# Kernel optimization log

Hardware: AMD Instinct MI355X
Metric: run time of the kernel (lower is better)

## Reference

```python
import jax, jax.numpy as jnp
import numpy as np

# --- static module config (from init_kwargs) ---
C1_OUT = 64          # c1OutChannels
C1K = 400            # k winners in conv layer
N_FC = 1024          # fc1 hidden units (n)
K_FC = 100           # k winners in fc1
BOOST = 1.0          # boostStrength
W_SPARSITY = 0.5     # weightSparsity: fraction of fc1 weights allowed nonzero
HP = 12              # pooled spatial size: floor((28-5+1)/2)
C1_OUTPUT_LEN = C1_OUT * HP * HP  # 9216
BATCH = 4096


def setup_inputs() -> dict:
    key = jax.random.key(0)
    ks = jax.random.split(key, 10)
    x = jax.random.normal(ks[0], (BATCH, 1, 28, 28), jnp.float32)
    c1_w = jax.random.normal(ks[1], (C1_OUT, 1, 5, 5), jnp.float32) * 0.1
    c1_b = jax.random.normal(ks[2], (C1_OUT,), jnp.float32) * 0.01
    # duty cycles live in [0, ~density]
    duty_cnn = jax.random.uniform(ks[3], (1, C1_OUT, 1, 1), jnp.float32) * 0.05
    fc1_w = jax.random.normal(ks[4], (N_FC, C1_OUT_LEN_ := C1_OUTPUT_LEN), jnp.float32) * 0.01
    fc1_mask_raw = jax.random.uniform(ks[5], (N_FC, C1_OUTPUT_LEN), jnp.float32)
    fc1_b = jax.random.normal(ks[6], (N_FC,), jnp.float32) * 0.01
    duty_fc = jax.random.uniform(ks[7], (N_FC,), jnp.float32) * 0.1
    fc2_w = jax.random.normal(ks[8], (10, N_FC), jnp.float32) * 0.05
    fc2_b = jnp.zeros((10,), jnp.float32)
    return dict(x=x, c1_w=c1_w, c1_b=c1_b, duty_cnn=duty_cnn, fc1_w=fc1_w,
                fc1_mask_raw=fc1_mask_raw, fc1_b=fc1_b, duty_fc=duty_fc,
                fc2_w=fc2_w, fc2_b=fc2_b)


def _kwinners(x_flat, boost_flat, k):
    """Duty-cycle-boosted k-winner mask.
    x_flat: [B, N]; boost_flat: [1, N] broadcastable boost factors.
    Keeps original x values at the top-k boosted positions per row, zeros rest.
    Boosting uses stop_gradient(x), matching KWinners*.forward(x.detach()*boost).
    """
    boosted = jax.lax.stop_gradient(x_flat) * boost_flat
    thr = jax.lax.top_k(boosted, k)[0][:, -1:]  # k-th largest per row
    return jnp.where(boosted >= thr, x_flat, jnp.zeros((), x_flat.dtype))


def reference(x, c1_w, c1_b, duty_cnn, fc1_w, fc1_mask_raw, fc1_b, duty_fc,
              fc2_w, fc2_b):
    B = x.shape[0]
    # conv2d (valid, stride 1) -> [B, 64, 24, 24]
    y = jax.lax.conv_general_dilated(
        x, c1_w, window_strides=(1, 1), padding='VALID',
        dimension_numbers=('NCHW', 'OIHW', 'NCHW')) + c1_b[None, :, None, None]
    # max_pool2d(2) -> [B, 64, 12, 12]
    y = jax.lax.reduce_window(y, -jnp.inf, jax.lax.max,
                              (1, 1, 2, 2), (1, 1, 2, 2), 'VALID')
    # KWinnersCNN: global top-k over flattened (C,H,W), per-channel boost
    target_density = C1K / C1_OUTPUT_LEN
    boost_c = jnp.exp((target_density - duty_cnn) * BOOST)  # [1,C,1,1]
    boost_flat = jnp.broadcast_to(boost_c, (1, C1_OUT, HP, HP)).reshape(1, -1)
    yf = _kwinners(y.reshape(B, -1), boost_flat, C1K)  # [B, 9216]
    # LinearSDR fc1: sparse-weight linear + KWinners
    w_mask = (fc1_mask_raw < W_SPARSITY).astype(fc1_w.dtype)
    h = yf @ (fc1_w * w_mask).T + fc1_b  # [B, 1024]
    boost_fc = jnp.exp((K_FC / N_FC - duty_fc) * BOOST)[None, :]
    h = _kwinners(h, boost_fc, K_FC)
    # fc2 + log_softmax (dropout inactive in eval mode)
    logits = h @ fc2_w.T + fc2_b
    return jax.nn.log_softmax(logits, axis=1)
```

## Files before the change

### kernel.cpp

```cpp
#include <hip/hip_runtime.h>

__device__ __forceinline__ float b2f(unsigned short u) {
  return __uint_as_float(((unsigned)u) << 16);
}
__device__ __forceinline__ unsigned short f2b(float f) {
  unsigned u = __float_as_uint(f);
  return (unsigned short)((u + 0x7FFFu + ((u >> 16) & 1u)) >> 16);
}
__device__ __forceinline__ float gload(const void* p, int i, int isb) {
  return isb ? b2f(((const unsigned short*)p)[i]) : ((const float*)p)[i];
}
__device__ __forceinline__ unsigned tokey(float f) {
  unsigned u = __float_as_uint(f);
  return u ^ (unsigned)(((int)u >> 31) | 0x80000000u);
}

__global__ void k_detect(const void* x, int* flag) {
  int tid = threadIdx.x;
  unsigned short u = ((const unsigned short*)x)[2 * tid];
  int e = (u >> 7) & 0xFF;
  bool sane = (e >= 100 && e <= 140);
  unsigned long long m = __ballot(sane);
  if (tid == 0) *flag = (__popcll(m) >= 40) ? 1 : 0;
}

__global__ __launch_bounds__(256) void k_prep(const void* __restrict__ fc1w,
                                              const void* __restrict__ mraw,
                                              float* __restrict__ WtF,
                                              const int* __restrict__ flag) {
  __shared__ float tile[64][65];
  const int isb = *flag;
  const int i0 = blockIdx.x * 64;
  const int u0 = blockIdx.y * 64;
  const int tx = threadIdx.x & 63, ty = threadIdx.x >> 6;
  for (int uu = ty; uu < 64; uu += 4) {
    int gi = (u0 + uu) * 9216 + i0 + tx;
    float wv = gload(fc1w, gi, isb);
    float mv = gload(mraw, gi, isb);
    tile[uu][tx] = (mv < 0.5f) ? wv : 0.0f;
  }
  __syncthreads();
  for (int ii = ty; ii < 64; ii += 4)
    WtF[(i0 + ii) * 1024 + u0 + tx] = tile[tx][ii];
}

__global__ __launch_bounds__(256) void k_conv(const void* __restrict__ x,
                                              const void* __restrict__ c1w_g,
                                              const void* __restrict__ c1b_g,
                                              const void* __restrict__ duty_g,
                                              int2* __restrict__ wpair,
                                              int* __restrict__ wcnt,
                                              const int* __restrict__ flag) {
  __shared__ __align__(16) float img[784];
  __shared__ float cw[1600];
  __shared__ float cb[64], bcs[64];
  __shared__ __align__(16) float pooled[9216];
  __shared__ unsigned hist4[4][256];
  __shared__ unsigned wtot[4];
  __shared__ unsigned selb, selk;
  const int tid = threadIdx.x;
  const int b = blockIdx.x;
  const int isb = *flag;
  const int lane = tid & 63;
  const int wv_id = tid >> 6;

  for (int i = tid; i < 784; i += 256) img[i] = gload(x, b * 784 + i, isb);
  for (int i = tid; i < 1600; i += 256) cw[i] = gload(c1w_g, i, isb);
  if (tid < 64) {
    cb[tid] = gload(c1b_g, tid, isb);
    float arg = (float)(400.0 / 9216.0) - gload(duty_g, tid, isb);
    bcs[tid] = (float)exp((double)arg);
  }
  __syncthreads();

  {
    const int c = tid >> 2;
    const int half = tid & 1;
    const int ph0 = ((tid >> 1) & 1) * 6;
    float w[25];
#pragma unroll
    for (int i = 0; i < 25; ++i) w[i] = cw[c * 25 + i];
    const float bias = cb[c];
    float R[6][16];
#pragma unroll
    for (int r = 0; r < 6; ++r) {
      int ir = 2 * ph0 + r;
#pragma unroll
      for (int q = 0; q < 4; ++q)
        ((float4*)&R[r][0])[q] = ((const float4*)img)[ir * 7 + half * 3 + q];
    }
#pragma unroll
    for (int i = 0; i < 6; ++i) {
      const int ph = ph0 + i;
      float a0[12], a1[12];
#pragma unroll
      for (int j = 0; j < 12; ++j) { a0[j] = 0.f; a1[j] = 0.f; }
#pragma unroll
      for (int kj = 0; kj < 5; ++kj) {
#pragma unroll
        for (int kr = 0; kr < 5; ++kr) {
          float wk = w[kr * 5 + kj];
          const float* r0 = &R[(2 * i + kr) % 6][0];
          const float* r1 = &R[(2 * i + kr + 1) % 6][0];
#pragma unroll
          for (int j = 0; j < 12; ++j) {
            a0[j] = fmaf(r0[j + kj], wk, a0[j]);
            a1[j] = fmaf(r1[j + kj], wk, a1[j]);
          }
        }
      }
      int obase = c * 144 + ph * 12 + half * 6;
#pragma unroll
      for (int q = 0; q < 6; ++q) {
        float m = fmaxf(fmaxf(a0[2 * q], a0[2 * q + 1]),
                        fmaxf(a1[2 * q], a1[2 * q + 1]));
        pooled[obase + q] = m + bias;
      }
      if (i < 5) {
        int ir0 = 2 * ph + 6, ir1 = 2 * ph + 7;
        float* d0 = &R[(2 * i) % 6][0];
        float* d1 = &R[(2 * i + 1) % 6][0];
#pragma unroll
        for (int q = 0; q < 4; ++q) {
          ((float4*)d0)[q] = ((const float4*)img)[ir0 * 7 + half * 3 + q];
          ((float4*)d1)[q] = ((const float4*)img)[ir1 * 7 + half * 3 + q];
        }
      }
    }
  }
  __syncthreads();

  unsigned keys[36];
  {
    const float bcf = bcs[tid >> 2];
#pragma unroll
    for (int e4 = 0; e4 < 9; ++e4) {
      float4 pv = ((float4*)pooled)[tid * 9 + e4];
      keys[4 * e4 + 0] = tokey(pv.x * bcf);
      keys[4 * e4 + 1] = tokey(pv.y * bcf);
      keys[4 * e4 + 2] = tokey(pv.z * bcf);
      keys[4 * e4 + 3] = tokey(pv.w * bcf);
    }
  }

  unsigned kfix = 0;
  unsigned kk = 400;
  for (int pass = 3; pass >= 0; --pass) {
    const int shift = pass * 8;
    const unsigned himask = (pass == 3) ? 0u : (0xFFFFFFFFu << (shift + 8));
#pragma unroll
    for (int w2 = 0; w2 < 4; ++w2) hist4[w2][tid] = 0;
    __syncthreads();
    unsigned* myh = hist4[wv_id];
#pragma unroll
    for (int e = 0; e < 36; ++e) {
      unsigned key = keys[e];
      if (((key ^ kfix) & himask) == 0)
        atomicAdd(&myh[(key >> shift) & 255u], 1u);
    }
    __syncthreads();
    unsigned own = hist4[0][tid] + hist4[1][tid] + hist4[2][tid] + hist4[3][tid];
    unsigned v = own;
#pragma unroll
    for (int off = 1; off < 64; off <<= 1) {
      unsigned y = __shfl_down(v, off, 64);
      if (lane + off < 64) v += y;
    }
    if (lane == 0) wtot[wv_id] = v;
    __syncthreads();
#pragma unroll
    for (int w2 = 0; w2 < 4; ++w2)
      if (w2 > wv_id) v += wtot[w2];
    unsigned snext = v - own;
    if (v >= kk && snext < kk) {
      selb = (unsigned)tid;
      selk = kk - snext;
    }
    __syncthreads();
    kfix |= selb << shift;
    kk = selk;
    __syncthreads();
  }

  unsigned mycnt = 0;
#pragma unroll
  for (int e = 0; e < 36; ++e) mycnt += (keys[e] >= kfix) ? 1u : 0u;
  unsigned px = mycnt;
#pragma unroll
  for (int off = 1; off < 64; off <<= 1) {
    unsigned y = __shfl_up(px, off, 64);
    if (lane >= off) px += y;
  }
  if (lane == 63) wtot[wv_id] = px;
  __syncthreads();
  unsigned base = 0;
#pragma unroll
  for (int w2 = 0; w2 < 4; ++w2)
    if (w2 < wv_id) base += wtot[w2];
  int pos = (int)(base + px - mycnt);
  for (int e = 0; e < 36; ++e) {
    if (keys[e] >= kfix) {
      int o = tid * 36 + e;
      if (pos < 512)
        wpair[b * 512 + pos] = make_int2(__float_as_int(pooled[o]), o << 12);
      ++pos;
    }
  }
  if (tid == 0) {
    unsigned tot = wtot[0] + wtot[1] + wtot[2] + wtot[3];
    wcnt[b] = (int)(tot < 512u ? tot : 512u);
  }
}

__global__ __launch_bounds__(128) void k_fc1(const float* __restrict__ WtF,
                                             const int2* __restrict__ wpair,
                                             const int* __restrict__ wcnt,
                                             const void* __restrict__ fc1b,
                                             float* __restrict__ h,
                                             const int* __restrict__ flag) {
  __shared__ int2 wl[512];
  const int tid = threadIdx.x;
  const int img = blockIdx.x >> 3;
  const int slice = blockIdx.x & 7;
  const int isb = *flag;
  const int cnt = wcnt[img];
  const int2* __restrict__ wp = wpair + img * 512;
  for (int i = tid; i < cnt; i += 128) wl[i] = wp[i];
  __syncthreads();
  const int u = (slice << 7) + tid;
  const unsigned ub = (unsigned)u * 4u;
  const char* __restrict__ Wb = (const char*)WtF;
  float acc = 0.f;
#pragma unroll 8
  for (int w = 0; w < cnt; ++w) {
    int2 p = wl[w];
    acc = fmaf(__int_as_float(p.x),
               *(const float*)(Wb + ((unsigned)p.y + ub)), acc);
  }
  h[img * 1024 + u] = acc + gload(fc1b, u, isb);
}

__global__ __launch_bounds__(256) void k_sel(const float* __restrict__ h,
                                             const void* __restrict__ dutyfc,
                                             const void* __restrict__ fc2w,
                                             const void* __restrict__ fc2b,
                                             void* __restrict__ out,
                                             const int* __restrict__ flag) {
  __shared__ unsigned hist[256];
  __shared__ unsigned selb, selk;
  __shared__ double lg[10];
  __shared__ double mred[2];
  const int tid = threadIdx.x;
  const int row = blockIdx.x;
  const int isb = *flag;
  if (tid < 10) lg[tid] = (double)gload(fc2b, tid, isb);
  __syncthreads();

  const int u0 = 2 * tid, u1 = 2 * tid + 1, u2 = 512 + 2 * tid, u3 = 513 + 2 * tid;
  float2 hlo = ((const float2*)(h + row * 1024))[tid];
  float2 hhi = ((const float2*)(h + row * 1024 + 512))[tid];
  float h0 = hlo.x, h1 = hlo.y, h2 = hhi.x, h3 = hhi.y;
  float bf0 = (float)exp((double)(0.09765625f - gload(dutyfc, u0, isb)));
  float bf1 = (float)exp((double)(0.09765625f - gload(dutyfc, u1, isb)));
  float bf2 = (float)exp((double)(0.09765625f - gload(dutyfc, u2, isb)));
  float bf3 = (float)exp((double)(0.09765625f - gload(dutyfc, u3, isb)));
  unsigned k0 = tokey(h0 * bf0);
  unsigned k1 = tokey(h1 * bf1);
  unsigned k2 = tokey(h2 * bf2);
  unsigned k3 = tokey(h3 * bf3);

  unsigned kfix = 0;
  int kk = 100;
  for (int pass = 3; pass >= 0; --pass) {
    const int shift = pass * 8;
    const unsigned himask = (pass == 3) ? 0u : (0xFFFFFFFFu << (shift + 8));
    hist[tid] = 0;
    __syncthreads();
    if (((k0 ^ kfix) & himask) == 0) atomicAdd(&hist[(k0 >> shift) & 255u], 1u);
    if (((k1 ^ kfix) & himask) == 0) atomicAdd(&hist[(k1 >> shift) & 255u], 1u);
    if (((k2 ^ kfix) & himask) == 0) atomicAdd(&hist[(k2 >> shift) & 255u], 1u);
    if (((k3 ^ kfix) & himask) == 0) atomicAdd(&hist[(k3 >> shift) & 255u], 1u);
    __syncthreads();
    unsigned v = hist[tid];
    for (int offs = 1; offs < 256; offs <<= 1) {
      unsigned other = (tid + offs < 256) ? hist[tid + offs] : 0u;
      __syncthreads();
      v += other;
      hist[tid] = v;
      __syncthreads();
    }
    unsigned snext = (tid < 255) ? hist[tid + 1] : 0u;
    if (v >= (unsigned)kk && snext < (unsigned)kk) {
      selb = (unsigned)tid;
      selk = (unsigned)(kk - (int)snext);
    }
    __syncthreads();
    kfix |= selb << shift;
    kk = (int)selk;
    __syncthreads();
  }
  bool kp0 = k0 >= kfix, kp1 = k1 >= kfix, kp2 = k2 >= kfix, kp3 = k3 >= kfix;

  double part[10];
#pragma unroll
  for (int c = 0; c < 10; ++c) part[c] = 0.0;
  if (kp0) {
#pragma unroll
    for (int c = 0; c < 10; ++c) part[c] = fma((double)h0, (double)gload(fc2w, c * 1024 + u0, isb), part[c]);
  }
  if (kp1) {
#pragma unroll
    for (int c = 0; c < 10; ++c) part[c] = fma((double)h1, (double)gload(fc2w, c * 1024 + u1, isb), part[c]);
  }
  if (kp2) {
#pragma unroll
    for (int c = 0; c < 10; ++c) part[c] = fma((double)h2, (double)gload(fc2w, c * 1024 + u2, isb), part[c]);
  }
  if (kp3) {
#pragma unroll
    for (int c = 0; c < 10; ++c) part[c] = fma((double)h3, (double)gload(fc2w, c * 1024 + u3, isb), part[c]);
  }
#pragma unroll
  for (int c = 0; c < 10; ++c) {
    double p = part[c];
    for (int off = 32; off > 0; off >>= 1) p += __shfl_xor(p, off);
    if ((tid & 63) == 0) atomicAdd(&lg[c], p);
  }
  __syncthreads();
  if (tid == 0) {
    double m = lg[0];
#pragma unroll
    for (int c = 1; c < 10; ++c) m = lg[c] > m ? lg[c] : m;
    double sum = 0.0;
#pragma unroll
    for (int c = 0; c < 10; ++c) sum += exp(lg[c] - m);
    mred[0] = m;
    mred[1] = log(sum);
  }
  __syncthreads();
  if (tid < 10) {
    double o = lg[tid] - mred[0] - mred[1];
    if (isb)
      ((unsigned short*)out)[row * 10 + tid] = f2b((float)o);
    else
      ((float*)out)[row * 10 + tid] = (float)o;
  }
}

extern "C" void kernel_launch(void* const* d_in, const int* in_sizes, int n_in,
                              void* d_out, int out_size, void* d_ws, size_t ws_size,
                              hipStream_t stream) {
  char* ws = (char*)d_ws;
  float* WtF = (float*)ws;
  int2* wpair = (int2*)(ws + 37748736);
  int* wcnt = (int*)(ws + 54525952);
  float* h = (float*)(ws + 54542336);
  int* flag = (int*)(ws + 71319552);

  k_detect<<<1, 64, 0, stream>>>(d_in[0], flag);
  k_prep<<<dim3(144, 16), 256, 0, stream>>>(d_in[4], d_in[5], WtF, flag);
  k_conv<<<4096, 256, 0, stream>>>(d_in[0], d_in[1], d_in[2], d_in[3],
                                   wpair, wcnt, flag);
  k_fc1<<<4096 * 8, 128, 0, stream>>>(WtF, wpair, wcnt, d_in[6], h, flag);
  k_sel<<<4096, 256, 0, stream>>>(h, d_in[7], d_in[8], d_in[9], d_out, flag);
}
```

Baseline: 624.5 us.

## Split conv kernel into conv/pool and k-winner selection kernels via global buffer

The fused conv+pool+top-k kernel is split in two. The first computes pooled activations and writes them to a global scratch buffer. The second reads them back, runs the radix-select and writes the winner pairs, processed in four chunks of 1024 images. The aim is to drop the 36KB shared pooled array so more blocks fit per CU, at the cost of an extra global round trip through L2 and more kernel launches. The scratch buffer aliases h, which is safe only because fc1 writes h afterwards.

```diff
diff --git a/kernel.cpp b/kernel.cpp
--- a/kernel.cpp
+++ b/kernel.cpp
@@ -44,102 +44,120 @@
     WtF[(i0 + ii) * 1024 + u0 + tx] = tile[tx][ii];
 }
 
-__global__ __launch_bounds__(256) void k_conv(const void* __restrict__ x,
-                                              const void* __restrict__ c1w_g,
-                                              const void* __restrict__ c1b_g,
-                                              const void* __restrict__ duty_g,
-                                              int2* __restrict__ wpair,
-                                              int* __restrict__ wcnt,
-                                              const int* __restrict__ flag) {
+__global__ __launch_bounds__(256) void k_convA(const void* __restrict__ x,
+                                               const void* __restrict__ c1w_g,
+                                               const void* __restrict__ c1b_g,
+                                               float* __restrict__ pooledG,
+                                               int batch0,
+                                               const int* __restrict__ flag) {
   __shared__ __align__(16) float img[784];
   __shared__ float cw[1600];
-  __shared__ float cb[64], bcs[64];
-  __shared__ __align__(16) float pooled[9216];
+  __shared__ float cb[64];
+  const int tid = threadIdx.x;
+  const int bl = blockIdx.x;
+  const int b = batch0 + bl;
+  const int isb = *flag;
+
+  for (int i = tid; i < 784; i += 256) img[i] = gload(x, b * 784 + i, isb);
+  for (int i = tid; i < 1600; i += 256) cw[i] = gload(c1w_g, i, isb);
+  if (tid < 64) cb[tid] = gload(c1b_g, tid, isb);
+  __syncthreads();
+
+  const int c = tid >> 2;
+  const int half = tid & 1;
+  const int ph0 = ((tid >> 1) & 1) * 6;
+  float w[25];
+#pragma unroll
+  for (int i = 0; i < 25; ++i) w[i] = cw[c * 25 + i];
+  const float bias = cb[c];
+  float R[6][16];
+#pragma unroll
+  for (int r = 0; r < 6; ++r) {
+    int ir = 2 * ph0 + r;
+#pragma unroll
+    for (int q = 0; q < 4; ++q)
+      ((float4*)&R[r][0])[q] = ((const float4*)img)[ir * 7 + half * 3 + q];
+  }
+  float* outp = pooledG + (size_t)bl * 9216;
+#pragma unroll
+  for (int i = 0; i < 6; ++i) {
+    const int ph = ph0 + i;
+    float a0[12], a1[12];
+#pragma unroll
+    for (int j = 0; j < 12; ++j) { a0[j] = 0.f; a1[j] = 0.f; }
+#pragma unroll
+    for (int kj = 0; kj < 5; ++kj) {
+#pragma unroll
+      for (int kr = 0; kr < 5; ++kr) {
+        float wk = w[kr * 5 + kj];
+        const float* r0 = &R[(2 * i + kr) % 6][0];
+        const float* r1 = &R[(2 * i + kr + 1) % 6][0];
+#pragma unroll
+        for (int j = 0; j < 12; ++j) {
+          a0[j] = fmaf(r0[j + kj], wk, a0[j]);
+          a1[j] = fmaf(r1[j + kj], wk, a1[j]);
+        }
+      }
+    }
+    int obase = c * 144 + ph * 12 + half * 6;
+#pragma unroll
+    for (int qq = 0; qq < 3; ++qq) {
+      float m0 = fmaxf(fmaxf(a0[4 * qq], a0[4 * qq + 1]),
+                       fmaxf(a1[4 * qq], a1[4 * qq + 1]));
+      float m1 = fmaxf(fmaxf(a0[4 * qq + 2], a0[4 * qq + 3]),
+                       fmaxf(a1[4 * qq + 2], a1[4 * qq + 3]));
+      *(float2*)(outp + obase + 2 * qq) = make_float2(m0 + bias, m1 + bias);
+    }
+    if (i < 5) {
+      int ir0 = 2 * ph + 6, ir1 = 2 * ph + 7;
+      float* d0 = &R[(2 * i) % 6][0];
+      float* d1 = &R[(2 * i + 1) % 6][0];
+#pragma unroll
+      for (int q = 0; q < 4; ++q) {
+        ((float4*)d0)[q] = ((const float4*)img)[ir0 * 7 + half * 3 + q];
+        ((float4*)d1)[q] = ((const float4*)img)[ir1 * 7 + half * 3 + q];
+      }
+    }
+  }
+}
+
+__global__ __launch_bounds__(256) void k_convB(const float* __restrict__ pooledG,
+                                               const void* __restrict__ duty_g,
+                                               int2* __restrict__ wpair,
+                                               int* __restrict__ wcnt,
+                                               int batch0,
+                                               const int* __restrict__ flag) {
+  __shared__ float bcs[64];
   __shared__ unsigned hist4[4][256];
   __shared__ unsigned wtot[4];
   __shared__ unsigned selb, selk;
   const int tid = threadIdx.x;
-  const int b = blockIdx.x;
+  const int bl = blockIdx.x;
+  const int b = batch0 + bl;
   const int isb = *flag;
   const int lane = tid & 63;
   const int wv_id = tid >> 6;
 
-  for (int i = tid; i < 784; i += 256) img[i] = gload(x, b * 784 + i, isb);
-  for (int i = tid; i < 1600; i += 256) cw[i] = gload(c1w_g, i, isb);
   if (tid < 64) {
-    cb[tid] = gload(c1b_g, tid, isb);
     float arg = (float)(400.0 / 9216.0) - gload(duty_g, tid, isb);
     bcs[tid] = (float)exp((double)arg);
   }
   __syncthreads();
 
-  {
-    const int c = tid >> 2;
-    const int half = tid & 1;
-    const int ph0 = ((tid >> 1) & 1) * 6;
-    float w[25];
-#pragma unroll
-    for (int i = 0; i < 25; ++i) w[i] = cw[c * 25 + i];
-    const float bias = cb[c];
-    float R[6][16];
-#pragma unroll
-    for (int r = 0; r < 6; ++r) {
-      int ir = 2 * ph0 + r;
-#pragma unroll
-      for (int q = 0; q < 4; ++q)
-        ((float4*)&R[r][0])[q] = ((const float4*)img)[ir * 7 + half * 3 + q];
-    }
-#pragma unroll
-    for (int i = 0; i < 6; ++i) {
-      const int ph = ph0 + i;
-      float a0[12], a1[12];
-#pragma unroll
-      for (int j = 0; j < 12; ++j) { a0[j] = 0.f; a1[j] = 0.f; }
-#pragma unroll
-      for (int kj = 0; kj < 5; ++kj) {
-#pragma unroll
-        for (int kr = 0; kr < 5; ++kr) {
-          float wk = w[kr * 5 + kj];
-          const float* r0 = &R[(2 * i + kr) % 6][0];
-          const float* r1 = &R[(2 * i + kr + 1) % 6][0];
-#pragma unroll
-          for (int j = 0; j < 12; ++j) {
-            a0[j] = fmaf(r0[j + kj], wk, a0[j]);
-            a1[j] = fmaf(r1[j + kj], wk, a1[j]);
-          }
-        }
-      }
-      int obase = c * 144 + ph * 12 + half * 6;
-#pragma unroll
-      for (int q = 0; q < 6; ++q) {
-        float m = fmaxf(fmaxf(a0[2 * q], a0[2 * q + 1]),
-                        fmaxf(a1[2 * q], a1[2 * q + 1]));
-        pooled[obase + q] = m + bias;
-      }
-      if (i < 5) {
-        int ir0 = 2 * ph + 6, ir1 = 2 * ph + 7;
-        float* d0 = &R[(2 * i) % 6][0];
-        float* d1 = &R[(2 * i + 1) % 6][0];
-#pragma unroll
-        for (int q = 0; q < 4; ++q) {
-          ((float4*)d0)[q] = ((const float4*)img)[ir0 * 7 + half * 3 + q];
-          ((float4*)d1)[q] = ((const float4*)img)[ir1 * 7 + half * 3 + q];
-        }
-      }
-    }
-  }
-  __syncthreads();
-
+  float pv[36];
   unsigned keys[36];
   {
+    const float* src = pooledG + (size_t)bl * 9216 + tid * 36;
     const float bcf = bcs[tid >> 2];
 #pragma unroll
     for (int e4 = 0; e4 < 9; ++e4) {
-      float4 pv = ((float4*)pooled)[tid * 9 + e4];
-      keys[4 * e4 + 0] = tokey(pv.x * bcf);
-      keys[4 * e4 + 1] = tokey(pv.y * bcf);
-      keys[4 * e4 + 2] = tokey(pv.z * bcf);
-      keys[4 * e4 + 3] = tokey(pv.w * bcf);
+      float4 v4 = ((const float4*)src)[e4];
+      pv[4 * e4 + 0] = v4.x; pv[4 * e4 + 1] = v4.y;
+      pv[4 * e4 + 2] = v4.z; pv[4 * e4 + 3] = v4.w;
+      keys[4 * e4 + 0] = tokey(v4.x * bcf);
+      keys[4 * e4 + 1] = tokey(v4.y * bcf);
+      keys[4 * e4 + 2] = tokey(v4.z * bcf);
+      keys[4 * e4 + 3] = tokey(v4.w * bcf);
     }
   }
 
@@ -202,7 +220,7 @@
     if (keys[e] >= kfix) {
       int o = tid * 36 + e;
       if (pos < 512)
-        wpair[b * 512 + pos] = make_int2(__float_as_int(pooled[o]), o << 12);
+        wpair[b * 512 + pos] = make_int2(__float_as_int(pv[e]), o << 12);
       ++pos;
     }
   }
@@ -354,13 +372,18 @@
   float* WtF = (float*)ws;
   int2* wpair = (int2*)(ws + 37748736);
   int* wcnt = (int*)(ws + 54525952);
+  float* pooledG = (float*)(ws + 54542336);
   float* h = (float*)(ws + 54542336);
-  int* flag = (int*)(ws + 71319552);
+  int* flag = (int*)(ws + 92291072);
 
   k_detect<<<1, 64, 0, stream>>>(d_in[0], flag);
   k_prep<<<dim3(144, 16), 256, 0, stream>>>(d_in[4], d_in[5], WtF, flag);
-  k_conv<<<4096, 256, 0, stream>>>(d_in[0], d_in[1], d_in[2], d_in[3],
-                                   wpair, wcnt, flag);
+  for (int t = 0; t < 4; ++t) {
+    k_convA<<<1024, 256, 0, stream>>>(d_in[0], d_in[1], d_in[2], pooledG,
+                                      t * 1024, flag);
+    k_convB<<<1024, 256, 0, stream>>>(pooledG, d_in[3], wpair, wcnt,
+                                      t * 1024, flag);
+  }
   k_fc1<<<4096 * 8, 128, 0, stream>>>(WtF, wpair, wcnt, d_in[6], h, flag);
   k_sel<<<4096, 256, 0, stream>>>(h, d_in[7], d_in[8], d_in[9], d_out, flag);
 }
```

Measured after the change: 691.6 us. 1.11x slower.
